# Kernel optimization log

Hardware: AMD Instinct MI355X
Metric: run time of the kernel (lower is better)

The kernel has to match this reference:

```python
import jax, jax.numpy as jnp
import numpy as np

N = 50000
E = 600000
NFEAT = 128
NHID = 128
PAD_N = 60000


def setup_inputs() -> dict:
    key = jax.random.key(0)
    ks = jax.random.split(key, 10)
    x = jax.random.normal(ks[0], (N, NFEAT), dtype=jnp.float32)
    edge_index = jax.random.randint(ks[1], (2, E), 0, N, dtype=jnp.int64)
    pos_idx = jnp.arange(N, dtype=jnp.int64)
    # SAGEConv params: lin_l (applied to mean-aggregated neighbors, with bias),
    # lin_r (applied to root/self features, no bias). Two layers.
    s1 = 1.0 / np.sqrt(NFEAT)
    s2 = 1.0 / np.sqrt(NHID)
    Wl1 = jax.random.uniform(ks[2], (NFEAT, NHID), jnp.float32, -s1, s1)
    Wr1 = jax.random.uniform(ks[3], (NFEAT, NHID), jnp.float32, -s1, s1)
    b1 = jax.random.uniform(ks[4], (NHID,), jnp.float32, -s1, s1)
    Wl2 = jax.random.uniform(ks[5], (NHID, NHID), jnp.float32, -s2, s2)
    Wr2 = jax.random.uniform(ks[6], (NHID, NHID), jnp.float32, -s2, s2)
    b2 = jax.random.uniform(ks[7], (NHID,), jnp.float32, -s2, s2)
    return {"x": x, "edge_index": edge_index, "pos_idx": pos_idx, "pad_n": PAD_N,
            "Wl1": Wl1, "Wr1": Wr1, "b1": b1, "Wl2": Wl2, "Wr2": Wr2, "b2": b2}


def _sage_conv(h, src, dst, Wl, Wr, b):
    # mean aggregation of source features into destination nodes
    msg = h[src]                                              # [E, F]
    agg = jax.ops.segment_sum(msg, dst, num_segments=N)       # [N, F]
    cnt = jax.ops.segment_sum(jnp.ones((dst.shape[0],), h.dtype), dst, num_segments=N)
    agg = agg / jnp.maximum(cnt, 1.0)[:, None]
    return agg @ Wl + h @ Wr + b


def reference(x, edge_index, pos_idx, pad_n, Wl1, Wr1, b1, Wl2, Wr2, b2):
    src, dst = edge_index[0], edge_index[1]
    h = jax.nn.relu(_sage_conv(x, src, dst, Wl1, Wr1, b1))
    # dropout is a no-op in eval mode (training=False)
    h = jax.nn.relu(_sage_conv(h, src, dst, Wl2, Wr2, b2))
    out = jnp.zeros((pad_n, h.shape[1]), h.dtype).at[pos_idx].set(h)
    return out
```

## Files before the change

kernel.cpp:

```cpp
#include <hip/hip_runtime.h>


#define NF 128
#define CAP 48

typedef _Float16 f16x8 __attribute__((ext_vector_type(8)));
typedef _Float16 f16x4 __attribute__((ext_vector_type(4)));
typedef float f32x4 __attribute__((ext_vector_type(4)));
typedef unsigned short u16;

__device__ __forceinline__ void swizzle_w(const float* __restrict__ Wl,
                                          const float* __restrict__ Wr,
                                          _Float16* __restrict__ Wf, int t) {
    int lane = t & 63;
    int frag = t >> 6;
    int s = frag >> 3, c = frag & 7;
    int n = s * 16 + (lane & 15);
    int kbase = c * 32 + (lane >> 4) * 8;
    f16x8 v;
#pragma unroll
    for (int j = 0; j < 8; ++j) {
        int k = kbase + j;
        float f = (k < NF) ? Wl[k * NF + n] : Wr[(k - NF) * NF + n];
        v[j] = (_Float16)f;
    }
    ((f16x8*)Wf)[frag * 64 + lane] = v;
}

__global__ void front_kernel(const int* __restrict__ src, const int* __restrict__ dst,
                             int* __restrict__ deg, u16* __restrict__ csr, int E,
                             const float* __restrict__ Wl1, const float* __restrict__ Wr1,
                             _Float16* __restrict__ Wf1,
                             const float* __restrict__ Wl2, const float* __restrict__ Wr2,
                             _Float16* __restrict__ Wf2,
                             const float4* __restrict__ x4, f16x4* __restrict__ xh4, int n4x,
                             float4* __restrict__ tail, int n4tail) {
    int nbf = (E / 4 + 255) >> 8;
    int nbc = (n4x + 255) >> 8;
    int b = blockIdx.x;
    if (b < nbf) {
        int e0 = (b * 256 + threadIdx.x) * 4;
        if (e0 + 4 <= E) {
            int4 d4 = *(const int4*)(dst + e0);
            int4 s4 = *(const int4*)(src + e0);
            int sl0 = atomicAdd(&deg[d4.x], 1);
            int sl1 = atomicAdd(&deg[d4.y], 1);
            int sl2 = atomicAdd(&deg[d4.z], 1);
            int sl3 = atomicAdd(&deg[d4.w], 1);
            if (sl0 < CAP) csr[(size_t)d4.x * CAP + sl0] = (u16)s4.x;
            if (sl1 < CAP) csr[(size_t)d4.y * CAP + sl1] = (u16)s4.y;
            if (sl2 < CAP) csr[(size_t)d4.z * CAP + sl2] = (u16)s4.z;
            if (sl3 < CAP) csr[(size_t)d4.w * CAP + sl3] = (u16)s4.w;
        } else {
            for (int e = e0; e < E; ++e) {
                int d = dst[e];
                int slot = atomicAdd(&deg[d], 1);
                if (slot < CAP) csr[(size_t)d * CAP + slot] = (u16)src[e];
            }
        }
    } else if (b < nbf + 16) {
        swizzle_w(Wl1, Wr1, Wf1, (b - nbf) * 256 + threadIdx.x);
    } else if (b < nbf + 32) {
        swizzle_w(Wl2, Wr2, Wf2, (b - nbf - 16) * 256 + threadIdx.x);
    } else if (b < nbf + 32 + nbc) {
        int i = (b - nbf - 32) * 256 + threadIdx.x;
        if (i < n4x) {
            float4 v = x4[i];
            f16x4 o;
            o[0] = (_Float16)v.x; o[1] = (_Float16)v.y;
            o[2] = (_Float16)v.z; o[3] = (_Float16)v.w;
            xh4[i] = o;
        }
    } else {
        int i = (b - nbf - 32 - nbc) * 256 + threadIdx.x;
        if (i < n4tail) tail[i] = make_float4(0.f, 0.f, 0.f, 0.f);
    }
}

#define LDA 136
template <bool LAST>
__global__ __launch_bounds__(256) void sage_layer_fused(
    const u16* __restrict__ csr, const int* __restrict__ deg,
    const _Float16* __restrict__ H,
    const _Float16* __restrict__ Wf,
    const float* __restrict__ bias,
    const int* __restrict__ pos,
    _Float16* __restrict__ outh,
    float* __restrict__ outf,
    int Nn) {
    __shared__ _Float16 sA[16][LDA];

    const int wave = threadIdx.x >> 6;
    const int lane = threadIdx.x & 63;
    const int sub  = lane >> 4;
    const int li   = lane & 15;
    const int m0 = blockIdx.x * 16;

    {
        int n = m0 + wave * 4 + sub;
        float a[8] = {0.f, 0.f, 0.f, 0.f, 0.f, 0.f, 0.f, 0.f};
        float b[8] = {0.f, 0.f, 0.f, 0.f, 0.f, 0.f, 0.f, 0.f};
        float inv = 1.0f;
        if (n < Nn) {
            int dg = deg[n];
            int rs = n * CAP;
            int re = rs + ((dg < CAP) ? dg : CAP);
            const f16x8* Hp = (const f16x8*)H;
            int k = rs;
            for (; k + 4 <= re; k += 4) {
                ushort4 c4 = *(const ushort4*)(csr + k);
                f16x8 v0 = Hp[(size_t)c4.x * 16 + li];
                f16x8 v1 = Hp[(size_t)c4.y * 16 + li];
                f16x8 v2 = Hp[(size_t)c4.z * 16 + li];
                f16x8 v3 = Hp[(size_t)c4.w * 16 + li];
#pragma unroll
                for (int j = 0; j < 8; ++j) {
                    a[j] += (float)v0[j] + (float)v2[j];
                    b[j] += (float)v1[j] + (float)v3[j];
                }
            }
            if (k + 2 <= re) {
                f16x8 v0 = Hp[(size_t)csr[k] * 16 + li];
                f16x8 v1 = Hp[(size_t)csr[k + 1] * 16 + li];
#pragma unroll
                for (int j = 0; j < 8; ++j) { a[j] += (float)v0[j]; b[j] += (float)v1[j]; }
                k += 2;
            }
            if (k < re) {
                f16x8 v0 = Hp[(size_t)csr[k] * 16 + li];
#pragma unroll
                for (int j = 0; j < 8; ++j) a[j] += (float)v0[j];
            }
            inv = 1.0f / fmaxf((float)dg, 1.0f);
        }
        f16x8 r;
#pragma unroll
        for (int j = 0; j < 8; ++j) r[j] = (_Float16)((a[j] + b[j]) * inv);
        *(f16x8*)&sA[wave * 4 + sub][li * 8] = r;
    }

    f16x8 bfrag[2][8];
    const f16x8* wfp = (const f16x8*)Wf;
#pragma unroll
    for (int s = 0; s < 2; ++s)
#pragma unroll
        for (int c = 0; c < 8; ++c)
            bfrag[s][c] = wfp[((2 * wave + s) * 8 + c) * 64 + lane];

    __syncthreads();

    f32x4 acc[2] = {(f32x4){0.f, 0.f, 0.f, 0.f}, (f32x4){0.f, 0.f, 0.f, 0.f}};

#pragma unroll
    for (int c = 0; c < 4; ++c) {
        f16x8 af = *(const f16x8*)&sA[li][c * 32 + sub * 8];
        acc[0] = __builtin_amdgcn_mfma_f32_16x16x32_f16(af, bfrag[0][c], acc[0], 0, 0, 0);
        acc[1] = __builtin_amdgcn_mfma_f32_16x16x32_f16(af, bfrag[1][c], acc[1], 0, 0, 0);
    }
    {
        int nd = m0 + li; if (nd >= Nn) nd = Nn - 1;
        const _Float16* xrow = H + (size_t)nd * NF;
#pragma unroll
        for (int c = 0; c < 4; ++c) {
            f16x8 af = *(const f16x8*)(xrow + c * 32 + sub * 8);
            acc[0] = __builtin_amdgcn_mfma_f32_16x16x32_f16(af, bfrag[0][4 + c], acc[0], 0, 0, 0);
            acc[1] = __builtin_amdgcn_mfma_f32_16x16x32_f16(af, bfrag[1][4 + c], acc[1], 0, 0, 0);
        }
    }

#pragma unroll
    for (int s = 0; s < 2; ++s) {
        int feat = (2 * wave + s) * 16 + li;
        float bv = bias[feat];
#pragma unroll
        for (int r = 0; r < 4; ++r) {
            int node = m0 + sub * 4 + r;
            if (node < Nn) {
                float v = fmaxf(acc[s][r] + bv, 0.f);
                if (LAST) outf[(size_t)pos[node] * NF + feat] = v;
                else      outh[(size_t)node * NF + feat] = (_Float16)v;
            }
        }
    }
}

extern "C" void kernel_launch(void* const* d_in, const int* in_sizes, int n_in,
                              void* d_out, int out_size, void* d_ws, size_t ws_size,
                              hipStream_t stream) {
    const float* x   = (const float*)d_in[0];
    const int*   ei  = (const int*)d_in[1];
    const int*   pos = (const int*)d_in[2];
    const float* Wl1 = (const float*)d_in[4];
    const float* Wr1 = (const float*)d_in[5];
    const float* b1  = (const float*)d_in[6];
    const float* Wl2 = (const float*)d_in[7];
    const float* Wr2 = (const float*)d_in[8];
    const float* b2  = (const float*)d_in[9];
    float* out = (float*)d_out;

    const int Nn = in_sizes[0] / NF;
    const int E  = in_sizes[1] / 2;
    const int* src = ei;
    const int* dst = ei + E;
    const int pad_rows = out_size / NF;

    const int degN = (Nn + 3) & ~3;
    _Float16* xh   = (_Float16*)d_ws;
    _Float16* h1h  = xh + (size_t)Nn * NF;
    _Float16* Wf1  = h1h + (size_t)Nn * NF;
    _Float16* Wf2  = Wf1 + 64 * 64 * 8;
    int* deg       = (int*)(Wf2 + 64 * 64 * 8);
    u16* csr       = (u16*)(deg + degN);

    const int ZB = 256;

    hipMemsetAsync(deg, 0, (size_t)degN * sizeof(int), stream);

    int n4x = Nn * NF / 4;
    int n4tail = (pad_rows - Nn) * NF / 4;
    int nbf = (E / 4 + ZB - 1) / ZB;
    int nbc = (n4x + ZB - 1) / ZB;
    int nbt = (n4tail + ZB - 1) / ZB;
    front_kernel<<<nbf + 32 + nbc + nbt, ZB, 0, stream>>>(
        src, dst, deg, csr, E,
        Wl1, Wr1, Wf1, Wl2, Wr2, Wf2,
        (const float4*)x, (f16x4*)xh, n4x,
        (float4*)(out + (size_t)Nn * NF), n4tail);

    const int fblocks = (Nn + 15) / 16;
    sage_layer_fused<false><<<fblocks, ZB, 0, stream>>>(
        csr, deg, xh, Wf1, b1, nullptr, h1h, nullptr, Nn);
    sage_layer_fused<true><<<fblocks, ZB, 0, stream>>>(
        csr, deg, h1h, Wf2, b2, pos, nullptr, out, Nn);
}
```

Measured before the change: 210.1 us.

## Merge both SAGE layers into one persistent kernel with a grid barrier

Replaces the two per-layer launches with a single persistent kernel of 512 blocks. Each block loops over 16-node tiles, loads its weight fragments once per layer, and meets the other blocks at a global atomic barrier between layers. The aim is to cut launch overhead and the tail gap between layers, and to stop reloading B fragments for every tile. The cost is lower occupancy (launch_bounds 256,2 and a fixed grid), less latency hiding for the irregular gathers, and a deadlock risk if all 512 blocks are not resident at the same time.

```diff
diff --git a/kernel.cpp b/kernel.cpp
--- a/kernel.cpp
+++ b/kernel.cpp
@@ -79,22 +79,12 @@
 
 #define LDA 136
 template <bool LAST>
-__global__ __launch_bounds__(256) void sage_layer_fused(
-    const u16* __restrict__ csr, const int* __restrict__ deg,
-    const _Float16* __restrict__ H,
-    const _Float16* __restrict__ Wf,
-    const float* __restrict__ bias,
-    const int* __restrict__ pos,
-    _Float16* __restrict__ outh,
-    float* __restrict__ outf,
-    int Nn) {
-    __shared__ _Float16 sA[16][LDA];
-
-    const int wave = threadIdx.x >> 6;
-    const int lane = threadIdx.x & 63;
-    const int sub  = lane >> 4;
-    const int li   = lane & 15;
-    const int m0 = blockIdx.x * 16;
+__device__ __forceinline__ void layer_tile(
+    int m0, const u16* __restrict__ csr, const int* __restrict__ deg,
+    const _Float16* __restrict__ H, const f16x8 (&bfrag)[2][8],
+    const float* __restrict__ bias, const int* __restrict__ pos,
+    _Float16* __restrict__ outh, float* __restrict__ outf, int Nn,
+    _Float16 (*sA)[LDA], int wave, int lane, int sub, int li) {
 
     {
         int n = m0 + wave * 4 + sub;
@@ -139,14 +129,6 @@
         *(f16x8*)&sA[wave * 4 + sub][li * 8] = r;
     }
 
-    f16x8 bfrag[2][8];
-    const f16x8* wfp = (const f16x8*)Wf;
-#pragma unroll
-    for (int s = 0; s < 2; ++s)
-#pragma unroll
-        for (int c = 0; c < 8; ++c)
-            bfrag[s][c] = wfp[((2 * wave + s) * 8 + c) * 64 + lane];
-
     __syncthreads();
 
     f32x4 acc[2] = {(f32x4){0.f, 0.f, 0.f, 0.f}, (f32x4){0.f, 0.f, 0.f, 0.f}};
@@ -181,6 +163,61 @@
                 else      outh[(size_t)node * NF + feat] = (_Float16)v;
             }
         }
+    }
+
+    __syncthreads();
+}
+
+__global__ __launch_bounds__(256, 2) void layers_kernel(
+    const u16* __restrict__ csr, const int* __restrict__ deg,
+    const _Float16* __restrict__ xh, _Float16* __restrict__ h1h,
+    const _Float16* __restrict__ Wf1, const _Float16* __restrict__ Wf2,
+    const float* __restrict__ b1, const float* __restrict__ b2,
+    const int* __restrict__ pos, float* __restrict__ out,
+    int* __restrict__ bar, int Nn, int ntiles) {
+    __shared__ _Float16 sA[16][LDA];
+
+    const int wave = threadIdx.x >> 6;
+    const int lane = threadIdx.x & 63;
+    const int sub  = lane >> 4;
+    const int li   = lane & 15;
+
+    {
+        f16x8 bfrag[2][8];
+        const f16x8* wfp = (const f16x8*)Wf1;
+#pragma unroll
+        for (int s = 0; s < 2; ++s)
+#pragma unroll
+            for (int c = 0; c < 8; ++c)
+                bfrag[s][c] = wfp[((2 * wave + s) * 8 + c) * 64 + lane];
+        for (int t = blockIdx.x; t < ntiles; t += gridDim.x)
+            layer_tile<false>(t * 16, csr, deg, xh, bfrag, b1, nullptr,
+                              h1h, nullptr, Nn, sA, wave, lane, sub, li);
+    }
+
+    __threadfence();
+    __syncthreads();
+    if (threadIdx.x == 0) {
+        __hip_atomic_fetch_add(bar, 1, __ATOMIC_ACQ_REL, __HIP_MEMORY_SCOPE_AGENT);
+        while (__hip_atomic_load(bar, __ATOMIC_ACQUIRE, __HIP_MEMORY_SCOPE_AGENT)
+               < (int)gridDim.x) {
+            __builtin_amdgcn_s_sleep(8);
+        }
+    }
+    __syncthreads();
+    __threadfence();
+
+    {
+        f16x8 bfrag[2][8];
+        const f16x8* wfp = (const f16x8*)Wf2;
+#pragma unroll
+        for (int s = 0; s < 2; ++s)
+#pragma unroll
+            for (int c = 0; c < 8; ++c)
+                bfrag[s][c] = wfp[((2 * wave + s) * 8 + c) * 64 + lane];
+        for (int t = blockIdx.x; t < ntiles; t += gridDim.x)
+            layer_tile<true>(t * 16, csr, deg, h1h, bfrag, b2, pos,
+                             nullptr, out, Nn, sA, wave, lane, sub, li);
     }
 }
 
@@ -210,11 +247,12 @@
     _Float16* Wf1  = h1h + (size_t)Nn * NF;
     _Float16* Wf2  = Wf1 + 64 * 64 * 8;
     int* deg       = (int*)(Wf2 + 64 * 64 * 8);
-    u16* csr       = (u16*)(deg + degN);
+    int* bar       = deg + degN;
+    u16* csr       = (u16*)(bar + 4);
 
     const int ZB = 256;
 
-    hipMemsetAsync(deg, 0, (size_t)degN * sizeof(int), stream);
+    hipMemsetAsync(deg, 0, (size_t)(degN + 4) * sizeof(int), stream);
 
     int n4x = Nn * NF / 4;
     int n4tail = (pad_rows - Nn) * NF / 4;
@@ -227,9 +265,7 @@
         (const float4*)x, (f16x4*)xh, n4x,
         (float4*)(out + (size_t)Nn * NF), n4tail);
 
-    const int fblocks = (Nn + 15) / 16;
-    sage_layer_fused<false><<<fblocks, ZB, 0, stream>>>(
-        csr, deg, xh, Wf1, b1, nullptr, h1h, nullptr, Nn);
-    sage_layer_fused<true><<<fblocks, ZB, 0, stream>>>(
-        csr, deg, h1h, Wf2, b2, pos, nullptr, out, Nn);
-}
+    int ntiles = (Nn + 15) / 16;
+    layers_kernel<<<512, ZB, 0, stream>>>(
+        csr, deg, xh, h1h, Wf1, Wf2, b1, b2, pos, out, bar, Nn, ntiles);
+}
```

Result: slower. 371.1 us (+76.6%).
